# Kernel tuning notes

Measured on AMD Instinct MI355X. Metric: run time of the kernel, lower is better.

The kernel has to match this reference:

```python
import jax, jax.numpy as jnp
import numpy as np

N_PTS = 1_000_000
RES = 512
RANK = 48
OUT = 32
INIT_SCALE = 0.1


def _plane_sample(plane, gx, gy):
    """Bilinear grid_sample, align_corners=True, border padding.
    plane: [R, Res, Res] (R=rank); gx, gy: [N] in [-1,1] -> [R, N]."""
    res = plane.shape[-1]
    px = jnp.clip((gx + 1.0) * 0.5 * (res - 1), 0.0, res - 1.0)
    py = jnp.clip((gy + 1.0) * 0.5 * (res - 1), 0.0, res - 1.0)
    x0 = jnp.floor(px).astype(jnp.int32)
    y0 = jnp.floor(py).astype(jnp.int32)
    x1 = jnp.minimum(x0 + 1, res - 1)
    y1 = jnp.minimum(y0 + 1, res - 1)
    wx = px - x0.astype(px.dtype)
    wy = py - y0.astype(py.dtype)
    # gathers: [R, N] each
    v00 = plane[:, y0, x0]
    v01 = plane[:, y0, x1]
    v10 = plane[:, y1, x0]
    v11 = plane[:, y1, x1]
    return (v00 * (1 - wy) * (1 - wx) + v01 * (1 - wy) * wx
            + v10 * wy * (1 - wx) + v11 * wy * wx)


def _line_sample(line, gy):
    """Line is [R, Res] (width dim of size 1 collapses; x coord is 0 -> px=0).
    1-D linear interp along Res with gy in [-1,1] -> [R, N]."""
    res = line.shape[-1]
    py = jnp.clip((gy + 1.0) * 0.5 * (res - 1), 0.0, res - 1.0)
    y0 = jnp.floor(py).astype(jnp.int32)
    y1 = jnp.minimum(y0 + 1, res - 1)
    wy = py - y0.astype(py.dtype)
    return line[:, y0] * (1 - wy) + line[:, y1] * wy


def _geo_forward(coordinates, plane_xy, plane_xz, plane_yz,
                 line_z, line_y, line_x, proj_w, proj_b):
    coords = coordinates * 2.0 - 1.0  # [N, 3] in [-1, 1]
    cx, cy, cz = coords[:, 0], coords[:, 1], coords[:, 2]
    vm = (_plane_sample(plane_xy, cx, cy) * _line_sample(line_z, cz)
          + _plane_sample(plane_xz, cx, cz) * _line_sample(line_y, cy)
          + _plane_sample(plane_yz, cy, cz) * _line_sample(line_x, cx))  # [R, N]
    # projection: [N, R] @ [R, OUT] + b
    return vm.T @ proj_w.T + proj_b


def setup_inputs() -> dict:
    key = jax.random.key(0)
    ks = jax.random.split(key, 9)
    return {
        "coordinates": jax.random.uniform(ks[0], (N_PTS, 3), dtype=jnp.float32),
        "plane_xy": jax.random.normal(ks[1], (RANK, RES, RES), jnp.float32) * INIT_SCALE,
        "plane_xz": jax.random.normal(ks[2], (RANK, RES, RES), jnp.float32) * INIT_SCALE,
        "plane_yz": jax.random.normal(ks[3], (RANK, RES, RES), jnp.float32) * INIT_SCALE,
        "line_z": jax.random.normal(ks[4], (RANK, RES), jnp.float32) * INIT_SCALE,
        "line_y": jax.random.normal(ks[5], (RANK, RES), jnp.float32) * INIT_SCALE,
        "line_x": jax.random.normal(ks[6], (RANK, RES), jnp.float32) * INIT_SCALE,
        "proj_w": jax.random.normal(ks[7], (OUT, RANK), jnp.float32) * INIT_SCALE,
        "proj_b": jnp.zeros((OUT,), jnp.float32),
    }


def reference(coordinates, plane_xy, plane_xz, plane_yz,
              line_z, line_y, line_x, proj_w, proj_b):
    return _geo_forward(coordinates, plane_xy, plane_xz, plane_yz,
                        line_z, line_y, line_x, proj_w, proj_b)
```

## Files before the change

### kernel.cpp

```cpp
#include <hip/hip_runtime.h>
#include <stdint.h>

#define RES      512
#define TEXELS   (RES * RES)
#define NPTS     1000000
#define RANK     48
#define ODIM     32
#define PPB      64
#define VMS      52
#define OSTR     33
#define TT       128
#define TS       25
#define CELLS    32768

typedef unsigned int u32;
typedef float vf4 __attribute__((ext_vector_type(4)));

__device__ __forceinline__ float lobf(u32 u) { return __uint_as_float(u << 16); }
__device__ __forceinline__ float hibf(u32 u) { return __uint_as_float(u & 0xffff0000u); }

__device__ __forceinline__ float ntl(const float* p) {
    return __builtin_nontemporal_load(p);
}
__device__ __forceinline__ u32 ntlu(const u32* p) {
    return __builtin_nontemporal_load(p);
}

__device__ __forceinline__ u32 pkbf(float a, float b) {
    u32 x = __float_as_uint(a), y = __float_as_uint(b);
    u32 xr = (x + 0x7fffu + ((x >> 16) & 1u)) >> 16;
    u32 yr = (y + 0x7fffu + ((y >> 16) & 1u)) & 0xffff0000u;
    return xr | yr;
}

__device__ __forceinline__ u32 sprd5(u32 a) {
    a &= 31u;
    a = (a | (a << 8)) & 0x100Fu;
    a = (a | (a << 4)) & 0x10C3u;
    a = (a | (a << 2)) & 0x1249u;
    return a;
}
__device__ __forceinline__ u32 cellOf(float x, float y, float z) {
    u32 cx = (u32)fminf(fmaxf(x * 32.f, 0.f), 31.f);
    u32 cy = (u32)fminf(fmaxf(y * 32.f, 0.f), 31.f);
    u32 cz = (u32)fminf(fmaxf(z * 32.f, 0.f), 31.f);
    return sprd5(cx) | (sprd5(cy) << 1) | (sprd5(cz) << 2);
}

template <int TEXB>
__global__ __launch_bounds__(256) void transpose_planes(
    const float* __restrict__ p0, const float* __restrict__ p1,
    const float* __restrict__ p2, char* __restrict__ ws)
{
    __shared__ u32 lds[TT * TS + 8];

    int t = threadIdx.x;
    int base = blockIdx.x * TT;
    int plane = blockIdx.y;
    const float* src = (plane == 0) ? p0 : ((plane == 1) ? p1 : p2);

    int t7 = t & (TT - 1);
    int half = t >> 7;
#pragma unroll
    for (int j = 0; j < 12; ++j) {
        int d = half * 12 + j;
        float a = ntl(&src[(size_t)(2 * d) * TEXELS + base + t7]);
        float b = ntl(&src[(size_t)(2 * d + 1) * TEXELS + base + t7]);
        lds[t7 * TS + d] = pkbf(a, b);
    }
    __syncthreads();

    char* outp = ws + (size_t)plane * TEXELS * TEXB + (size_t)base * TEXB;
    constexpr int NS = TT * TEXB / (16 * 256);
#pragma unroll
    for (int s = 0; s < NS; ++s) {
        u32 o = (u32)(s * 256 + t) * 16u;
        u32 texel, rem;
        if (TEXB == 128) { texel = o >> 7; rem = o & 127u; }
        else {
            texel = ((o >> 5) * 43691u) >> 17;
            rem = o - texel * 96u;
        }
        u32 dw = texel * TS + (rem >> 2);
        uint4 q = make_uint4(lds[dw], lds[dw + 1], lds[dw + 2], lds[dw + 3]);
        *(uint4*)(outp + o) = q;
    }
}

template <int TEXB>
__global__ __launch_bounds__(256) void transpose_lines(
    const float* __restrict__ lz, const float* __restrict__ ly,
    const float* __restrict__ lx, char* __restrict__ ws)
{
    int id = blockIdx.x * 256 + threadIdx.x;
    int line = id >> 9;
    int pos = id & (RES - 1);
    const float* src = (line == 0) ? lz : ((line == 1) ? ly : lx);
    char* dst = ws + (size_t)3 * TEXELS * TEXB + (size_t)line * RES * TEXB
                   + (size_t)pos * TEXB;
#pragma unroll
    for (int k = 0; k < 6; ++k) {
        uint4 q;
        q.x = pkbf(ntl(&src[(8 * k + 0) * RES + pos]), ntl(&src[(8 * k + 1) * RES + pos]));
        q.y = pkbf(ntl(&src[(8 * k + 2) * RES + pos]), ntl(&src[(8 * k + 3) * RES + pos]));
        q.z = pkbf(ntl(&src[(8 * k + 4) * RES + pos]), ntl(&src[(8 * k + 5) * RES + pos]));
        q.w = pkbf(ntl(&src[(8 * k + 6) * RES + pos]), ntl(&src[(8 * k + 7) * RES + pos]));
        *(uint4*)(dst + 16 * k) = q;
    }
}

__global__ __launch_bounds__(256) void zero_counts(u32* __restrict__ counts) {
    counts[blockIdx.x * 256 + threadIdx.x] = 0u;
}

__global__ __launch_bounds__(256) void cell_count(
    const float* __restrict__ coords, u32* __restrict__ counts)
{
    int pt = blockIdx.x * 256 + threadIdx.x;
    if (pt >= NPTS) return;
    float x = ntl(&coords[3 * pt + 0]);
    float y = ntl(&coords[3 * pt + 1]);
    float z = ntl(&coords[3 * pt + 2]);
    atomicAdd(&counts[cellOf(x, y, z)], 1u);
}

__global__ __launch_bounds__(1024) void cell_scan(
    const u32* __restrict__ counts, u32* __restrict__ cursors)
{
    __shared__ u32 wt[16];
    int t = threadIdx.x;
    u32 local[32];
    u32 s = 0;
#pragma unroll
    for (int i = 0; i < 32; ++i) {
        local[i] = s;
        s += counts[t * 32 + i];
    }
    u32 tot = s;
    int lane = t & 63, w = t >> 6;
    u32 incl = tot;
#pragma unroll
    for (int d = 1; d < 64; d <<= 1) {
        u32 v = __shfl_up(incl, d);
        if (lane >= d) incl += v;
    }
    if (lane == 63) wt[w] = incl;
    __syncthreads();
    if (t == 0) {
        u32 a = 0;
#pragma unroll
        for (int i = 0; i < 16; ++i) { u32 x = wt[i]; wt[i] = a; a += x; }
    }
    __syncthreads();
    u32 base = wt[w] + (incl - tot);
#pragma unroll
    for (int i = 0; i < 32; ++i)
        cursors[t * 32 + i] = base + local[i];
}

__global__ __launch_bounds__(256) void cell_scatter(
    const float* __restrict__ coords, u32* __restrict__ cursors,
    u32* __restrict__ perm, float* __restrict__ rc)
{
    int pt = blockIdx.x * 256 + threadIdx.x;
    if (pt >= NPTS) return;
    float x = ntl(&coords[3 * pt + 0]);
    float y = ntl(&coords[3 * pt + 1]);
    float z = ntl(&coords[3 * pt + 2]);
    u32 pos = atomicAdd(&cursors[cellOf(x, y, z)], 1u);
    perm[pos] = (u32)pt;
    rc[3 * pos + 0] = x;
    rc[3 * pos + 1] = y;
    rc[3 * pos + 2] = z;
}

__device__ __forceinline__ void prep1(float g, int& i0, int& i1, float& w) {
    float p = fminf(fmaxf((g + 1.f) * 0.5f * 511.f, 0.f), 511.f);
    float fp = floorf(p);
    i0 = (int)fp;
    i1 = min(i0 + 1, RES - 1);
    w = p - fp;
}

template <int TEXB, bool SORTED>
__global__ __launch_bounds__(512, 4) void geo_main(
    const float* __restrict__ coords, const char* __restrict__ ws,
    const u32* __restrict__ perm,
    const float* __restrict__ W, const float* __restrict__ Bb,
    float* __restrict__ out)
{
    __shared__ float vm_lds[PPB * VMS];
    __shared__ u32 opt_lds[PPB];

    int tid = threadIdx.x;
    int ptL = tid >> 3;
    int c = tid & 7;

    int bid = blockIdx.x;
    if (SORTED) {
        int nwg = gridDim.x;
        int q = nwg >> 3, r = nwg & 7;
        int xcd = bid & 7, slot = bid >> 3;
        bid = (xcd < r ? xcd * (q + 1) : r * (q + 1) + (xcd - r) * q) + slot;
    }
    int pt = bid * PPB + ptL;

    float gx = ntl(&coords[3 * pt + 0]) * 2.f - 1.f;
    float gy = ntl(&coords[3 * pt + 1]) * 2.f - 1.f;
    float gz = ntl(&coords[3 * pt + 2]) * 2.f - 1.f;

    if (c == 0)
        opt_lds[ptL] = SORTED ? ntlu(&perm[pt]) : (u32)pt;

    int x0, x1, y0, y1, z0, z1;
    float wx, wy, wz;
    prep1(gx, x0, x1, wx);
    prep1(gy, y0, y1, wy);
    prep1(gz, z0, z1, wz);

    const size_t PW = (size_t)TEXELS * TEXB;
    const size_t LW = (size_t)RES * TEXB;
    const char* pxy = ws;
    const char* pxz = ws + PW;
    const char* pyz = ws + 2 * PW;
    const char* lzb = ws + 3 * PW;
    const char* lyb = lzb + LW;
    const char* lxb = lyb + LW;

    u32 co = 12u * (u32)c;

    u32 q[12][3], le[3][3], lf[3][3];
    {
        u32 offs[12];
        offs[0] = (u32)(y0 * RES + x0) * TEXB + co;
        offs[1] = (u32)(y0 * RES + x1) * TEXB + co;
        offs[2] = (u32)(y1 * RES + x0) * TEXB + co;
        offs[3] = (u32)(y1 * RES + x1) * TEXB + co;
        offs[4] = (u32)(z0 * RES + x0) * TEXB + co;
        offs[5] = (u32)(z0 * RES + x1) * TEXB + co;
        offs[6] = (u32)(z1 * RES + x0) * TEXB + co;
        offs[7] = (u32)(z1 * RES + x1) * TEXB + co;
        offs[8]  = (u32)(z0 * RES + y0) * TEXB + co;
        offs[9]  = (u32)(z0 * RES + y1) * TEXB + co;
        offs[10] = (u32)(z1 * RES + y0) * TEXB + co;
        offs[11] = (u32)(z1 * RES + y1) * TEXB + co;
        const char* bases[3] = { pxy, pxz, pyz };
#pragma unroll
        for (int p = 0; p < 3; ++p) {
#pragma unroll
            for (int k = 0; k < 4; ++k) {
                const u32* s = (const u32*)(bases[p] + offs[4 * p + k]);
                q[4 * p + k][0] = s[0];
                q[4 * p + k][1] = s[1];
                q[4 * p + k][2] = s[2];
            }
        }
        const char* lb[3] = { lzb, lyb, lxb };
        u32 l0[3] = { (u32)z0 * TEXB + co, (u32)y0 * TEXB + co, (u32)x0 * TEXB + co };
        u32 l1[3] = { (u32)z1 * TEXB + co, (u32)y1 * TEXB + co, (u32)x1 * TEXB + co };
#pragma unroll
        for (int p = 0; p < 3; ++p) {
            const u32* s0 = (const u32*)(lb[p] + l0[p]);
            const u32* s1 = (const u32*)(lb[p] + l1[p]);
            le[p][0] = s0[0]; le[p][1] = s0[1]; le[p][2] = s0[2];
            lf[p][0] = s1[0]; lf[p][1] = s1[1]; lf[p][2] = s1[2];
        }
    }

    float pw[3][4];
    pw[0][0] = (1.f - wy) * (1.f - wx); pw[0][1] = (1.f - wy) * wx;
    pw[0][2] = wy * (1.f - wx);         pw[0][3] = wy * wx;
    pw[1][0] = (1.f - wz) * (1.f - wx); pw[1][1] = (1.f - wz) * wx;
    pw[1][2] = wz * (1.f - wx);         pw[1][3] = wz * wx;
    pw[2][0] = (1.f - wz) * (1.f - wy); pw[2][1] = (1.f - wz) * wy;
    pw[2][2] = wz * (1.f - wy);         pw[2][3] = wz * wy;
    float lw[3] = { wz, wy, wx };

    float vm[6] = { 0.f, 0.f, 0.f, 0.f, 0.f, 0.f };
#pragma unroll
    for (int p = 0; p < 3; ++p) {
        float s0 = pw[p][0], s1 = pw[p][1], s2 = pw[p][2], s3 = pw[p][3];
        float il = 1.f - lw[p], wl = lw[p];
#pragma unroll
        for (int d = 0; d < 3; ++d) {
            u32 a = q[4 * p + 0][d], b = q[4 * p + 1][d];
            u32 cc = q[4 * p + 2][d], dd = q[4 * p + 3][d];
            float slo = s0 * lobf(a) + s1 * lobf(b) + s2 * lobf(cc) + s3 * lobf(dd);
            float shi = s0 * hibf(a) + s1 * hibf(b) + s2 * hibf(cc) + s3 * hibf(dd);
            float llo = il * lobf(le[p][d]) + wl * lobf(lf[p][d]);
            float lhi = il * hibf(le[p][d]) + wl * hibf(lf[p][d]);
            vm[2 * d + 0] = fmaf(slo, llo, vm[2 * d + 0]);
            vm[2 * d + 1] = fmaf(shi, lhi, vm[2 * d + 1]);
        }
    }

    float* vr = vm_lds + ptL * VMS + 6 * c;
    *(float2*)(vr + 0) = make_float2(vm[0], vm[1]);
    *(float2*)(vr + 2) = make_float2(vm[2], vm[3]);
    *(float2*)(vr + 4) = make_float2(vm[4], vm[5]);

    __syncthreads();

    int wav = __builtin_amdgcn_readfirstlane(tid >> 6);
    int lane = tid & 63;
    int ob = wav * 4;

    const float* vmrow = vm_lds + lane * VMS;
    float4 bb = *(const float4*)(Bb + ob);
    float a0 = bb.x, a1 = bb.y, a2 = bb.z, a3 = bb.w;
#pragma unroll 4
    for (int k = 0; k < 12; ++k) {
        float4 v = *(const float4*)(vmrow + 4 * k);
        float4 w0 = *(const float4*)(W + (ob + 0) * RANK + 4 * k);
        float4 w1 = *(const float4*)(W + (ob + 1) * RANK + 4 * k);
        float4 w2 = *(const float4*)(W + (ob + 2) * RANK + 4 * k);
        float4 w3 = *(const float4*)(W + (ob + 3) * RANK + 4 * k);
        a0 = fmaf(v.x, w0.x, a0); a0 = fmaf(v.y, w0.y, a0);
        a0 = fmaf(v.z, w0.z, a0); a0 = fmaf(v.w, w0.w, a0);
        a1 = fmaf(v.x, w1.x, a1); a1 = fmaf(v.y, w1.y, a1);
        a1 = fmaf(v.z, w1.z, a1); a1 = fmaf(v.w, w1.w, a1);
        a2 = fmaf(v.x, w2.x, a2); a2 = fmaf(v.y, w2.y, a2);
        a2 = fmaf(v.z, w2.z, a2); a2 = fmaf(v.w, w2.w, a2);
        a3 = fmaf(v.x, w3.x, a3); a3 = fmaf(v.y, w3.y, a3);
        a3 = fmaf(v.z, w3.z, a3); a3 = fmaf(v.w, w3.w, a3);
    }

    __syncthreads();
    {
        vf4 r; r.x = a0; r.y = a1; r.z = a2; r.w = a3;
        *(vf4*)(vm_lds + lane * OSTR + ob) = r;
    }
    __syncthreads();
    {
        int p8 = lane >> 3;
        int c2 = lane & 7;
        int gp = wav * 8 + p8;
        vf4 v = *(const vf4*)(vm_lds + gp * OSTR + 4 * c2);
        size_t orow = (size_t)opt_lds[gp];
        __builtin_nontemporal_store(v, (vf4*)(out + orow * ODIM + 4 * c2));
    }
}

template <int TEXB>
static void launch_unsorted(const float* coords, const float* pxy, const float* pxz,
                            const float* pyz, const float* lz, const float* ly,
                            const float* lx, const float* W, const float* Bb,
                            float* out, char* ws, hipStream_t stream) {
    dim3 gt(TEXELS / TT, 3);
    transpose_planes<TEXB><<<gt, 256, 0, stream>>>(pxy, pxz, pyz, ws);
    transpose_lines<TEXB><<<6, 256, 0, stream>>>(lz, ly, lx, ws);
    geo_main<TEXB, false><<<NPTS / PPB, 512, 0, stream>>>(coords, ws, nullptr, W, Bb, out);
}

extern "C" void kernel_launch(void* const* d_in, const int* in_sizes, int n_in,
                              void* d_out, int out_size, void* d_ws, size_t ws_size,
                              hipStream_t stream) {
    const float* coords = (const float*)d_in[0];
    const float* pxy = (const float*)d_in[1];
    const float* pxz = (const float*)d_in[2];
    const float* pyz = (const float*)d_in[3];
    const float* lz = (const float*)d_in[4];
    const float* ly = (const float*)d_in[5];
    const float* lx = (const float*)d_in[6];
    const float* W = (const float*)d_in[7];
    const float* Bb = (const float*)d_in[8];
    float* out = (float*)d_out;
    char* ws = (char*)d_ws;

    size_t pool96 = (size_t)3 * TEXELS * 96 + (size_t)3 * RES * 96;
    size_t o_counts = (pool96 + 255) & ~(size_t)255;
    size_t o_cursors = o_counts + (size_t)CELLS * 4;
    size_t o_perm = o_cursors + (size_t)CELLS * 4;
    size_t o_rc = o_perm + (size_t)NPTS * 4;
    size_t need_sorted = o_rc + (size_t)NPTS * 12;
    size_t need128 = (size_t)3 * TEXELS * 128 + (size_t)3 * RES * 128;
    size_t need96 = pool96;

    if (ws_size >= need_sorted) {
        u32* counts = (u32*)(ws + o_counts);
        u32* cursors = (u32*)(ws + o_cursors);
        u32* perm = (u32*)(ws + o_perm);
        float* rc = (float*)(ws + o_rc);

        dim3 gt(TEXELS / TT, 3);
        transpose_planes<96><<<gt, 256, 0, stream>>>(pxy, pxz, pyz, ws);
        transpose_lines<96><<<6, 256, 0, stream>>>(lz, ly, lx, ws);
        zero_counts<<<CELLS / 256, 256, 0, stream>>>(counts);
        cell_count<<<(NPTS + 255) / 256, 256, 0, stream>>>(coords, counts);
        cell_scan<<<1, 1024, 0, stream>>>(counts, cursors);
        cell_scatter<<<(NPTS + 255) / 256, 256, 0, stream>>>(coords, cursors, perm, rc);
        geo_main<96, true><<<NPTS / PPB, 512, 0, stream>>>(rc, ws, perm, W, Bb, out);
    } else if (ws_size >= need128) {
        launch_unsorted<128>(coords, pxy, pxz, pyz, lz, ly, lx, W, Bb, out, ws, stream);
    } else {
        launch_unsorted<96>(coords, pxy, pxz, pyz, lz, ly, lx, W, Bb, out, ws, stream);
    }
}
```

Measured before the change: 483.3 us.

## Fuse preprocessing kernels and overlap plane transpose with sort passes

Merges the plane transpose, line transpose, cell count, scan and scatter into three heterogeneous kernels. The transpose tiles are split across them so the transpose work runs alongside the latency-bound count, scan and scatter passes. The separate perm array and 12-byte coordinate buffer become one 16-byte record (xyz plus the original index), read with a single vector load in the main kernel. The zeroing kernel becomes a memset, the scan uses a single 256-thread block, and transpose loads are widened to float4. Launch count drops, at the cost of more complex kernels and a 16-byte rather than 12-byte workspace record per point.

After: 463.4 us. -4.1%, faster.

```diff
diff --git a/kernel.cpp b/kernel.cpp
--- a/kernel.cpp
+++ b/kernel.cpp
@@ -12,6 +12,11 @@
 #define TT       128
 #define TS       25
 #define CELLS    32768
+#define TPALL    6144
+#define TPA      2560
+#define TPB      512
+#define TPC      3072
+#define CNTB     3907
 
 typedef unsigned int u32;
 typedef float vf4 __attribute__((ext_vector_type(4)));
@@ -22,8 +27,8 @@
 __device__ __forceinline__ float ntl(const float* p) {
     return __builtin_nontemporal_load(p);
 }
-__device__ __forceinline__ u32 ntlu(const u32* p) {
-    return __builtin_nontemporal_load(p);
+__device__ __forceinline__ vf4 ntl4(const float* p) {
+    return __builtin_nontemporal_load((const vf4*)p);
 }
 
 __device__ __forceinline__ u32 pkbf(float a, float b) {
@@ -47,57 +52,48 @@
     return sprd5(cx) | (sprd5(cy) << 1) | (sprd5(cz) << 2);
 }
 
-template <int TEXB>
-__global__ __launch_bounds__(256) void transpose_planes(
+__device__ __forceinline__ void tp_role(int bx, int t,
     const float* __restrict__ p0, const float* __restrict__ p1,
-    const float* __restrict__ p2, char* __restrict__ ws)
-{
-    __shared__ u32 lds[TT * TS + 8];
-
-    int t = threadIdx.x;
-    int base = blockIdx.x * TT;
-    int plane = blockIdx.y;
+    const float* __restrict__ p2, char* __restrict__ ws, u32* lds)
+{
+    int tile = bx & 2047;
+    int plane = bx >> 11;
     const float* src = (plane == 0) ? p0 : ((plane == 1) ? p1 : p2);
-
-    int t7 = t & (TT - 1);
-    int half = t >> 7;
-#pragma unroll
-    for (int j = 0; j < 12; ++j) {
-        int d = half * 12 + j;
-        float a = ntl(&src[(size_t)(2 * d) * TEXELS + base + t7]);
-        float b = ntl(&src[(size_t)(2 * d + 1) * TEXELS + base + t7]);
-        lds[t7 * TS + d] = pkbf(a, b);
-    }
-    __syncthreads();
-
-    char* outp = ws + (size_t)plane * TEXELS * TEXB + (size_t)base * TEXB;
-    constexpr int NS = TT * TEXB / (16 * 256);
-#pragma unroll
-    for (int s = 0; s < NS; ++s) {
+    int base = tile * TT;
+    int xi = t & 31, dg = t >> 5;
+#pragma unroll
+    for (int j = 0; j < 3; ++j) {
+        int d = dg + 8 * j;
+        vf4 a = ntl4(src + (size_t)(2 * d) * TEXELS + base + 4 * xi);
+        vf4 b = ntl4(src + (size_t)(2 * d + 1) * TEXELS + base + 4 * xi);
+        lds[(4 * xi + 0) * TS + d] = pkbf(a.x, b.x);
+        lds[(4 * xi + 1) * TS + d] = pkbf(a.y, b.y);
+        lds[(4 * xi + 2) * TS + d] = pkbf(a.z, b.z);
+        lds[(4 * xi + 3) * TS + d] = pkbf(a.w, b.w);
+    }
+    __syncthreads();
+    char* outp = ws + (size_t)plane * TEXELS * 96 + (size_t)base * 96;
+#pragma unroll
+    for (int s = 0; s < 3; ++s) {
         u32 o = (u32)(s * 256 + t) * 16u;
-        u32 texel, rem;
-        if (TEXB == 128) { texel = o >> 7; rem = o & 127u; }
-        else {
-            texel = ((o >> 5) * 43691u) >> 17;
-            rem = o - texel * 96u;
-        }
+        u32 texel = ((o >> 5) * 43691u) >> 17;
+        u32 rem = o - texel * 96u;
         u32 dw = texel * TS + (rem >> 2);
         uint4 q = make_uint4(lds[dw], lds[dw + 1], lds[dw + 2], lds[dw + 3]);
         *(uint4*)(outp + o) = q;
     }
 }
 
-template <int TEXB>
-__global__ __launch_bounds__(256) void transpose_lines(
+__device__ __forceinline__ void lines_role(int lbx, int t,
     const float* __restrict__ lz, const float* __restrict__ ly,
     const float* __restrict__ lx, char* __restrict__ ws)
 {
-    int id = blockIdx.x * 256 + threadIdx.x;
+    int id = lbx * 256 + t;
     int line = id >> 9;
     int pos = id & (RES - 1);
     const float* src = (line == 0) ? lz : ((line == 1) ? ly : lx);
-    char* dst = ws + (size_t)3 * TEXELS * TEXB + (size_t)line * RES * TEXB
-                   + (size_t)pos * TEXB;
+    char* dst = ws + (size_t)3 * TEXELS * 96 + (size_t)line * RES * 96
+                   + (size_t)pos * 96;
 #pragma unroll
     for (int k = 0; k < 6; ++k) {
         uint4 q;
@@ -109,14 +105,10 @@
     }
 }
 
-__global__ __launch_bounds__(256) void zero_counts(u32* __restrict__ counts) {
-    counts[blockIdx.x * 256 + threadIdx.x] = 0u;
-}
-
-__global__ __launch_bounds__(256) void cell_count(
+__device__ __forceinline__ void count_role(int cbx, int t,
     const float* __restrict__ coords, u32* __restrict__ counts)
 {
-    int pt = blockIdx.x * 256 + threadIdx.x;
+    int pt = cbx * 256 + t;
     if (pt >= NPTS) return;
     float x = ntl(&coords[3 * pt + 0]);
     float y = ntl(&coords[3 * pt + 1]);
@@ -124,54 +116,138 @@
     atomicAdd(&counts[cellOf(x, y, z)], 1u);
 }
 
-__global__ __launch_bounds__(1024) void cell_scan(
-    const u32* __restrict__ counts, u32* __restrict__ cursors)
-{
-    __shared__ u32 wt[16];
-    int t = threadIdx.x;
-    u32 local[32];
-    u32 s = 0;
-#pragma unroll
-    for (int i = 0; i < 32; ++i) {
-        local[i] = s;
-        s += counts[t * 32 + i];
-    }
-    u32 tot = s;
-    int lane = t & 63, w = t >> 6;
+__device__ __forceinline__ void scan_role(int t,
+    const u32* __restrict__ counts, u32* __restrict__ cursors, u32* wt)
+{
+    const u32* cp = counts + t * 128;
+    u32 tot = 0;
+#pragma unroll 16
+    for (int i = 0; i < 128; ++i) tot += cp[i];
+    int lane = t & 63;
     u32 incl = tot;
 #pragma unroll
-    for (int d = 1; d < 64; d <<= 1) {
-        u32 v = __shfl_up(incl, d);
-        if (lane >= d) incl += v;
-    }
+    for (int d2 = 1; d2 < 64; d2 <<= 1) {
+        u32 v = __shfl_up(incl, d2);
+        if (lane >= d2) incl += v;
+    }
+    int w = t >> 6;
     if (lane == 63) wt[w] = incl;
     __syncthreads();
-    if (t == 0) {
-        u32 a = 0;
-#pragma unroll
-        for (int i = 0; i < 16; ++i) { u32 x = wt[i]; wt[i] = a; a += x; }
-    }
-    __syncthreads();
-    u32 base = wt[w] + (incl - tot);
-#pragma unroll
-    for (int i = 0; i < 32; ++i)
-        cursors[t * 32 + i] = base + local[i];
-}
-
-__global__ __launch_bounds__(256) void cell_scatter(
+    u32 run = incl - tot;
+#pragma unroll
+    for (int i = 0; i < 4; ++i) run += (i < w) ? wt[i] : 0u;
+    u32* op = cursors + t * 128;
+#pragma unroll 16
+    for (int i = 0; i < 128; ++i) { u32 c2 = cp[i]; op[i] = run; run += c2; }
+}
+
+__device__ __forceinline__ void scatter_role(int cbx, int t,
     const float* __restrict__ coords, u32* __restrict__ cursors,
-    u32* __restrict__ perm, float* __restrict__ rc)
-{
-    int pt = blockIdx.x * 256 + threadIdx.x;
+    vf4* __restrict__ rc2)
+{
+    int pt = cbx * 256 + t;
     if (pt >= NPTS) return;
     float x = ntl(&coords[3 * pt + 0]);
     float y = ntl(&coords[3 * pt + 1]);
     float z = ntl(&coords[3 * pt + 2]);
     u32 pos = atomicAdd(&cursors[cellOf(x, y, z)], 1u);
-    perm[pos] = (u32)pt;
-    rc[3 * pos + 0] = x;
-    rc[3 * pos + 1] = y;
-    rc[3 * pos + 2] = z;
+    vf4 v; v.x = x; v.y = y; v.z = z; v.w = __uint_as_float((u32)pt);
+    rc2[pos] = v;
+}
+
+__global__ __launch_bounds__(256) void k1_count_tp(
+    const float* __restrict__ coords, u32* __restrict__ counts,
+    const float* __restrict__ p0, const float* __restrict__ p1,
+    const float* __restrict__ p2, char* __restrict__ ws)
+{
+    __shared__ u32 lds[TT * TS + 8];
+    int bx = blockIdx.x, t = threadIdx.x;
+    if (bx < CNTB) count_role(bx, t, coords, counts);
+    else tp_role(bx - CNTB, t, p0, p1, p2, ws, lds);
+}
+
+__global__ __launch_bounds__(256) void k2_scan_lines_tp(
+    const u32* __restrict__ counts, u32* __restrict__ cursors,
+    const float* __restrict__ lz, const float* __restrict__ ly,
+    const float* __restrict__ lx,
+    const float* __restrict__ p0, const float* __restrict__ p1,
+    const float* __restrict__ p2, char* __restrict__ ws)
+{
+    __shared__ u32 lds[TT * TS + 8];
+    int bx = blockIdx.x, t = threadIdx.x;
+    if (bx == 0) scan_role(t, counts, cursors, lds);
+    else if (bx <= 6) lines_role(bx - 1, t, lz, ly, lx, ws);
+    else tp_role(bx - 7 + TPA, t, p0, p1, p2, ws, lds);
+}
+
+__global__ __launch_bounds__(256) void k3_scatter_tp(
+    const float* __restrict__ coords, u32* __restrict__ cursors,
+    vf4* __restrict__ rc2,
+    const float* __restrict__ p0, const float* __restrict__ p1,
+    const float* __restrict__ p2, char* __restrict__ ws)
+{
+    __shared__ u32 lds[TT * TS + 8];
+    int bx = blockIdx.x, t = threadIdx.x;
+    if (bx < CNTB) scatter_role(bx, t, coords, cursors, rc2);
+    else tp_role(bx - CNTB + TPA + TPB, t, p0, p1, p2, ws, lds);
+}
+
+template <int TEXB>
+__global__ __launch_bounds__(256) void transpose_planes(
+    const float* __restrict__ p0, const float* __restrict__ p1,
+    const float* __restrict__ p2, char* __restrict__ ws)
+{
+    __shared__ u32 lds[TT * TS + 8];
+    int t = threadIdx.x;
+    int base = blockIdx.x * TT;
+    int plane = blockIdx.y;
+    const float* src = (plane == 0) ? p0 : ((plane == 1) ? p1 : p2);
+    int xi = t & 31, dg = t >> 5;
+#pragma unroll
+    for (int j = 0; j < 3; ++j) {
+        int d = dg + 8 * j;
+        vf4 a = ntl4(src + (size_t)(2 * d) * TEXELS + base + 4 * xi);
+        vf4 b = ntl4(src + (size_t)(2 * d + 1) * TEXELS + base + 4 * xi);
+        lds[(4 * xi + 0) * TS + d] = pkbf(a.x, b.x);
+        lds[(4 * xi + 1) * TS + d] = pkbf(a.y, b.y);
+        lds[(4 * xi + 2) * TS + d] = pkbf(a.z, b.z);
+        lds[(4 * xi + 3) * TS + d] = pkbf(a.w, b.w);
+    }
+    __syncthreads();
+    char* outp = ws + (size_t)plane * TEXELS * TEXB + (size_t)base * TEXB;
+    constexpr int NS = TT * TEXB / (16 * 256);
+#pragma unroll
+    for (int s = 0; s < NS; ++s) {
+        u32 o = (u32)(s * 256 + t) * 16u;
+        u32 texel, rem;
+        if (TEXB == 128) { texel = o >> 7; rem = o & 127u; }
+        else { texel = ((o >> 5) * 43691u) >> 17; rem = o - texel * 96u; }
+        u32 dw = texel * TS + (rem >> 2);
+        uint4 q = make_uint4(lds[dw], lds[dw + 1], lds[dw + 2], lds[dw + 3]);
+        *(uint4*)(outp + o) = q;
+    }
+}
+
+template <int TEXB>
+__global__ __launch_bounds__(256) void transpose_lines(
+    const float* __restrict__ lz, const float* __restrict__ ly,
+    const float* __restrict__ lx, char* __restrict__ ws)
+{
+    int id = blockIdx.x * 256 + threadIdx.x;
+    int line = id >> 9;
+    int pos = id & (RES - 1);
+    const float* src = (line == 0) ? lz : ((line == 1) ? ly : lx);
+    char* dst = ws + (size_t)3 * TEXELS * TEXB + (size_t)line * RES * TEXB
+                   + (size_t)pos * TEXB;
+#pragma unroll
+    for (int k = 0; k < 6; ++k) {
+        uint4 q;
+        q.x = pkbf(ntl(&src[(8 * k + 0) * RES + pos]), ntl(&src[(8 * k + 1) * RES + pos]));
+        q.y = pkbf(ntl(&src[(8 * k + 2) * RES + pos]), ntl(&src[(8 * k + 3) * RES + pos]));
+        q.z = pkbf(ntl(&src[(8 * k + 4) * RES + pos]), ntl(&src[(8 * k + 5) * RES + pos]));
+        q.w = pkbf(ntl(&src[(8 * k + 6) * RES + pos]), ntl(&src[(8 * k + 7) * RES + pos]));
+        *(uint4*)(dst + 16 * k) = q;
+    }
 }
 
 __device__ __forceinline__ void prep1(float g, int& i0, int& i1, float& w) {
@@ -184,8 +260,7 @@
 
 template <int TEXB, bool SORTED>
 __global__ __launch_bounds__(512, 4) void geo_main(
-    const float* __restrict__ coords, const char* __restrict__ ws,
-    const u32* __restrict__ perm,
+    const void* __restrict__ cin, const char* __restrict__ ws,
     const float* __restrict__ W, const float* __restrict__ Bb,
     float* __restrict__ out)
 {
@@ -205,12 +280,20 @@
     }
     int pt = bid * PPB + ptL;
 
-    float gx = ntl(&coords[3 * pt + 0]) * 2.f - 1.f;
-    float gy = ntl(&coords[3 * pt + 1]) * 2.f - 1.f;
-    float gz = ntl(&coords[3 * pt + 2]) * 2.f - 1.f;
-
-    if (c == 0)
-        opt_lds[ptL] = SORTED ? ntlu(&perm[pt]) : (u32)pt;
+    float gx, gy, gz;
+    if (SORTED) {
+        vf4 cc = __builtin_nontemporal_load((const vf4*)cin + pt);
+        gx = cc.x * 2.f - 1.f;
+        gy = cc.y * 2.f - 1.f;
+        gz = cc.z * 2.f - 1.f;
+        if (c == 0) opt_lds[ptL] = __float_as_uint(cc.w);
+    } else {
+        const float* coords = (const float*)cin;
+        gx = ntl(&coords[3 * pt + 0]) * 2.f - 1.f;
+        gy = ntl(&coords[3 * pt + 1]) * 2.f - 1.f;
+        gz = ntl(&coords[3 * pt + 2]) * 2.f - 1.f;
+        if (c == 0) opt_lds[ptL] = (u32)pt;
+    }
 
     int x0, x1, y0, y1, z0, z1;
     float wx, wy, wz;
@@ -349,7 +432,7 @@
     dim3 gt(TEXELS / TT, 3);
     transpose_planes<TEXB><<<gt, 256, 0, stream>>>(pxy, pxz, pyz, ws);
     transpose_lines<TEXB><<<6, 256, 0, stream>>>(lz, ly, lx, ws);
-    geo_main<TEXB, false><<<NPTS / PPB, 512, 0, stream>>>(coords, ws, nullptr, W, Bb, out);
+    geo_main<TEXB, false><<<NPTS / PPB, 512, 0, stream>>>(coords, ws, W, Bb, out);
 }
 
 extern "C" void kernel_launch(void* const* d_in, const int* in_sizes, int n_in,
@@ -370,26 +453,24 @@
     size_t pool96 = (size_t)3 * TEXELS * 96 + (size_t)3 * RES * 96;
     size_t o_counts = (pool96 + 255) & ~(size_t)255;
     size_t o_cursors = o_counts + (size_t)CELLS * 4;
-    size_t o_perm = o_cursors + (size_t)CELLS * 4;
-    size_t o_rc = o_perm + (size_t)NPTS * 4;
-    size_t need_sorted = o_rc + (size_t)NPTS * 12;
+    size_t o_rc2 = o_cursors + (size_t)CELLS * 4;
+    size_t need_sorted = o_rc2 + (size_t)NPTS * 16;
     size_t need128 = (size_t)3 * TEXELS * 128 + (size_t)3 * RES * 128;
-    size_t need96 = pool96;
 
     if (ws_size >= need_sorted) {
         u32* counts = (u32*)(ws + o_counts);
         u32* cursors = (u32*)(ws + o_cursors);
-        u32* perm = (u32*)(ws + o_perm);
-        float* rc = (float*)(ws + o_rc);
-
-        dim3 gt(TEXELS / TT, 3);
-        transpose_planes<96><<<gt, 256, 0, stream>>>(pxy, pxz, pyz, ws);
-        transpose_lines<96><<<6, 256, 0, stream>>>(lz, ly, lx, ws);
-        zero_counts<<<CELLS / 256, 256, 0, stream>>>(counts);
-        cell_count<<<(NPTS + 255) / 256, 256, 0, stream>>>(coords, counts);
-        cell_scan<<<1, 1024, 0, stream>>>(counts, cursors);
-        cell_scatter<<<(NPTS + 255) / 256, 256, 0, stream>>>(coords, cursors, perm, rc);
-        geo_main<96, true><<<NPTS / PPB, 512, 0, stream>>>(rc, ws, perm, W, Bb, out);
+        vf4* rc2 = (vf4*)(ws + o_rc2);
+
+        hipMemsetAsync(counts, 0, (size_t)CELLS * 4, stream);
+        k1_count_tp<<<CNTB + TPA, 256, 0, stream>>>(coords, counts,
+                                                    pxy, pxz, pyz, ws);
+        k2_scan_lines_tp<<<7 + TPB, 256, 0, stream>>>(counts, cursors,
+                                                      lz, ly, lx,
+                                                      pxy, pxz, pyz, ws);
+        k3_scatter_tp<<<CNTB + TPC, 256, 0, stream>>>(coords, cursors, rc2,
+                                                      pxy, pxz, pyz, ws);
+        geo_main<96, true><<<NPTS / PPB, 512, 0, stream>>>(rc2, ws, W, Bb, out);
     } else if (ws_size >= need128) {
         launch_unsorted<128>(coords, pxy, pxz, pyz, lz, ly, lx, W, Bb, out, ws, stream);
     } else {
```

## Fuse prep kernels and pack sorted coords with point index

Applied to the files above, without the earlier changes.

The plane transpose, line transpose and cell counting are merged into one heterogeneous kernel whose blocks take different roles, so these independent preprocessing steps run concurrently and need fewer launches. The plane transpose no longer stages through LDS; each thread gathers 48 channels of one texel directly. The scatter writes a single 16-byte record (xyz plus original index) instead of separate perm and coordinate arrays, so the main kernel reads one vector load per point. Zeroing is done with a memset, and the 128-byte layout path is removed. Risks: the uncoalesced per-texel transpose reads and grid-stride loops could cost more than the saved launch overhead.

Result: no change. 474.8 us (-1.7%).

```diff
diff --git a/kernel.cpp b/kernel.cpp
--- a/kernel.cpp
+++ b/kernel.cpp
@@ -9,9 +9,11 @@
 #define PPB      64
 #define VMS      52
 #define OSTR     33
-#define TT       128
-#define TS       25
 #define CELLS    32768
+#define LINB     6
+#define CNTB     256
+#define TPB      1536
+#define SCTB     1024
 
 typedef unsigned int u32;
 typedef float vf4 __attribute__((ext_vector_type(4)));
@@ -20,9 +22,6 @@
 __device__ __forceinline__ float hibf(u32 u) { return __uint_as_float(u & 0xffff0000u); }
 
 __device__ __forceinline__ float ntl(const float* p) {
-    return __builtin_nontemporal_load(p);
-}
-__device__ __forceinline__ u32 ntlu(const u32* p) {
     return __builtin_nontemporal_load(p);
 }
 
@@ -47,57 +46,44 @@
     return sprd5(cx) | (sprd5(cy) << 1) | (sprd5(cz) << 2);
 }
 
-template <int TEXB>
-__global__ __launch_bounds__(256) void transpose_planes(
+__device__ __forceinline__ void tp_one(int g,
     const float* __restrict__ p0, const float* __restrict__ p1,
     const float* __restrict__ p2, char* __restrict__ ws)
 {
-    __shared__ u32 lds[TT * TS + 8];
-
-    int t = threadIdx.x;
-    int base = blockIdx.x * TT;
-    int plane = blockIdx.y;
+    int plane = g >> 18;
+    int texel = g & (TEXELS - 1);
     const float* src = (plane == 0) ? p0 : ((plane == 1) ? p1 : p2);
-
-    int t7 = t & (TT - 1);
-    int half = t >> 7;
-#pragma unroll
-    for (int j = 0; j < 12; ++j) {
-        int d = half * 12 + j;
-        float a = ntl(&src[(size_t)(2 * d) * TEXELS + base + t7]);
-        float b = ntl(&src[(size_t)(2 * d + 1) * TEXELS + base + t7]);
-        lds[t7 * TS + d] = pkbf(a, b);
-    }
-    __syncthreads();
-
-    char* outp = ws + (size_t)plane * TEXELS * TEXB + (size_t)base * TEXB;
-    constexpr int NS = TT * TEXB / (16 * 256);
-#pragma unroll
-    for (int s = 0; s < NS; ++s) {
-        u32 o = (u32)(s * 256 + t) * 16u;
-        u32 texel, rem;
-        if (TEXB == 128) { texel = o >> 7; rem = o & 127u; }
-        else {
-            texel = ((o >> 5) * 43691u) >> 17;
-            rem = o - texel * 96u;
-        }
-        u32 dw = texel * TS + (rem >> 2);
-        uint4 q = make_uint4(lds[dw], lds[dw + 1], lds[dw + 2], lds[dw + 3]);
-        *(uint4*)(outp + o) = q;
-    }
-}
-
-template <int TEXB>
-__global__ __launch_bounds__(256) void transpose_lines(
+    u32 c2[24];
+#pragma unroll
+    for (int h = 0; h < 2; ++h) {
+        float fa[12], fb[12];
+#pragma unroll
+        for (int d = 0; d < 12; ++d) {
+            fa[d] = ntl(src + (size_t)(2 * (h * 12 + d) + 0) * TEXELS + texel);
+            fb[d] = ntl(src + (size_t)(2 * (h * 12 + d) + 1) * TEXELS + texel);
+        }
+#pragma unroll
+        for (int d = 0; d < 12; ++d) c2[h * 12 + d] = pkbf(fa[d], fb[d]);
+    }
+    char* dst = ws + (size_t)plane * TEXELS * 96 + (size_t)texel * 96;
+#pragma unroll
+    for (int s = 0; s < 6; ++s) {
+        uint4 q = make_uint4(c2[4 * s + 0], c2[4 * s + 1],
+                             c2[4 * s + 2], c2[4 * s + 3]);
+        *(uint4*)(dst + 16 * s) = q;
+    }
+}
+
+__device__ __forceinline__ void lines_role(int j, int t,
     const float* __restrict__ lz, const float* __restrict__ ly,
     const float* __restrict__ lx, char* __restrict__ ws)
 {
-    int id = blockIdx.x * 256 + threadIdx.x;
+    int id = j * 256 + t;
     int line = id >> 9;
     int pos = id & (RES - 1);
     const float* src = (line == 0) ? lz : ((line == 1) ? ly : lx);
-    char* dst = ws + (size_t)3 * TEXELS * TEXB + (size_t)line * RES * TEXB
-                   + (size_t)pos * TEXB;
+    char* dst = ws + (size_t)3 * TEXELS * 96 + (size_t)line * RES * 96
+                   + (size_t)pos * 96;
 #pragma unroll
     for (int k = 0; k < 6; ++k) {
         uint4 q;
@@ -109,22 +95,31 @@
     }
 }
 
-__global__ __launch_bounds__(256) void zero_counts(u32* __restrict__ counts) {
-    counts[blockIdx.x * 256 + threadIdx.x] = 0u;
-}
-
-__global__ __launch_bounds__(256) void cell_count(
-    const float* __restrict__ coords, u32* __restrict__ counts)
-{
-    int pt = blockIdx.x * 256 + threadIdx.x;
-    if (pt >= NPTS) return;
-    float x = ntl(&coords[3 * pt + 0]);
-    float y = ntl(&coords[3 * pt + 1]);
-    float z = ntl(&coords[3 * pt + 2]);
-    atomicAdd(&counts[cellOf(x, y, z)], 1u);
-}
-
-__global__ __launch_bounds__(1024) void cell_scan(
+__global__ __launch_bounds__(256) void k1_prep(
+    const float* __restrict__ coords, u32* __restrict__ counts,
+    const float* __restrict__ p0, const float* __restrict__ p1,
+    const float* __restrict__ p2,
+    const float* __restrict__ lz, const float* __restrict__ ly,
+    const float* __restrict__ lx, char* __restrict__ ws)
+{
+    int bx = blockIdx.x, t = threadIdx.x;
+    if (bx < LINB) {
+        lines_role(bx, t, lz, ly, lx, ws);
+    } else if (bx < LINB + CNTB) {
+        for (int idx = (bx - LINB) * 256 + t; idx < NPTS; idx += CNTB * 256) {
+            float x = ntl(&coords[3 * idx + 0]);
+            float y = ntl(&coords[3 * idx + 1]);
+            float z = ntl(&coords[3 * idx + 2]);
+            atomicAdd(&counts[cellOf(x, y, z)], 1u);
+        }
+    } else {
+        int w = bx - LINB - CNTB;
+        for (int g = w * 256 + t; g < 3 * TEXELS; g += TPB * 256)
+            tp_one(g, p0, p1, p2, ws);
+    }
+}
+
+__global__ __launch_bounds__(1024) void k2_scan(
     const u32* __restrict__ counts, u32* __restrict__ cursors)
 {
     __shared__ u32 wt[16];
@@ -158,20 +153,33 @@
         cursors[t * 32 + i] = base + local[i];
 }
 
-__global__ __launch_bounds__(256) void cell_scatter(
+__global__ __launch_bounds__(256) void k3_scatter(
     const float* __restrict__ coords, u32* __restrict__ cursors,
-    u32* __restrict__ perm, float* __restrict__ rc)
-{
-    int pt = blockIdx.x * 256 + threadIdx.x;
-    if (pt >= NPTS) return;
-    float x = ntl(&coords[3 * pt + 0]);
-    float y = ntl(&coords[3 * pt + 1]);
-    float z = ntl(&coords[3 * pt + 2]);
-    u32 pos = atomicAdd(&cursors[cellOf(x, y, z)], 1u);
-    perm[pos] = (u32)pt;
-    rc[3 * pos + 0] = x;
-    rc[3 * pos + 1] = y;
-    rc[3 * pos + 2] = z;
+    vf4* __restrict__ rc2)
+{
+    int t = threadIdx.x;
+    for (int idx = blockIdx.x * 256 + t; idx < NPTS; idx += SCTB * 256) {
+        float x = ntl(&coords[3 * idx + 0]);
+        float y = ntl(&coords[3 * idx + 1]);
+        float z = ntl(&coords[3 * idx + 2]);
+        u32 pos = atomicAdd(&cursors[cellOf(x, y, z)], 1u);
+        vf4 v; v.x = x; v.y = y; v.z = z; v.w = __uint_as_float((u32)idx);
+        __builtin_nontemporal_store(v, rc2 + pos);
+    }
+}
+
+__global__ __launch_bounds__(256) void tp_stream_only(
+    const float* __restrict__ p0, const float* __restrict__ p1,
+    const float* __restrict__ p2, char* __restrict__ ws)
+{
+    int g = blockIdx.x * 256 + threadIdx.x;
+    tp_one(g, p0, p1, p2, ws);
+}
+__global__ __launch_bounds__(256) void lines_only(
+    const float* __restrict__ lz, const float* __restrict__ ly,
+    const float* __restrict__ lx, char* __restrict__ ws)
+{
+    lines_role(blockIdx.x, threadIdx.x, lz, ly, lx, ws);
 }
 
 __device__ __forceinline__ void prep1(float g, int& i0, int& i1, float& w) {
@@ -184,8 +192,7 @@
 
 template <int TEXB, bool SORTED>
 __global__ __launch_bounds__(512, 4) void geo_main(
-    const float* __restrict__ coords, const char* __restrict__ ws,
-    const u32* __restrict__ perm,
+    const void* __restrict__ cin, const char* __restrict__ ws,
     const float* __restrict__ W, const float* __restrict__ Bb,
     float* __restrict__ out)
 {
@@ -205,12 +212,20 @@
     }
     int pt = bid * PPB + ptL;
 
-    float gx = ntl(&coords[3 * pt + 0]) * 2.f - 1.f;
-    float gy = ntl(&coords[3 * pt + 1]) * 2.f - 1.f;
-    float gz = ntl(&coords[3 * pt + 2]) * 2.f - 1.f;
-
-    if (c == 0)
-        opt_lds[ptL] = SORTED ? ntlu(&perm[pt]) : (u32)pt;
+    float gx, gy, gz;
+    if (SORTED) {
+        vf4 cc = __builtin_nontemporal_load((const vf4*)cin + pt);
+        gx = cc.x * 2.f - 1.f;
+        gy = cc.y * 2.f - 1.f;
+        gz = cc.z * 2.f - 1.f;
+        if (c == 0) opt_lds[ptL] = __float_as_uint(cc.w);
+    } else {
+        const float* coords = (const float*)cin;
+        gx = ntl(&coords[3 * pt + 0]) * 2.f - 1.f;
+        gy = ntl(&coords[3 * pt + 1]) * 2.f - 1.f;
+        gz = ntl(&coords[3 * pt + 2]) * 2.f - 1.f;
+        if (c == 0) opt_lds[ptL] = (u32)pt;
+    }
 
     int x0, x1, y0, y1, z0, z1;
     float wx, wy, wz;
@@ -341,17 +356,6 @@
     }
 }
 
-template <int TEXB>
-static void launch_unsorted(const float* coords, const float* pxy, const float* pxz,
-                            const float* pyz, const float* lz, const float* ly,
-                            const float* lx, const float* W, const float* Bb,
-                            float* out, char* ws, hipStream_t stream) {
-    dim3 gt(TEXELS / TT, 3);
-    transpose_planes<TEXB><<<gt, 256, 0, stream>>>(pxy, pxz, pyz, ws);
-    transpose_lines<TEXB><<<6, 256, 0, stream>>>(lz, ly, lx, ws);
-    geo_main<TEXB, false><<<NPTS / PPB, 512, 0, stream>>>(coords, ws, nullptr, W, Bb, out);
-}
-
 extern "C" void kernel_launch(void* const* d_in, const int* in_sizes, int n_in,
                               void* d_out, int out_size, void* d_ws, size_t ws_size,
                               hipStream_t stream) {
@@ -370,29 +374,24 @@
     size_t pool96 = (size_t)3 * TEXELS * 96 + (size_t)3 * RES * 96;
     size_t o_counts = (pool96 + 255) & ~(size_t)255;
     size_t o_cursors = o_counts + (size_t)CELLS * 4;
-    size_t o_perm = o_cursors + (size_t)CELLS * 4;
-    size_t o_rc = o_perm + (size_t)NPTS * 4;
-    size_t need_sorted = o_rc + (size_t)NPTS * 12;
-    size_t need128 = (size_t)3 * TEXELS * 128 + (size_t)3 * RES * 128;
-    size_t need96 = pool96;
+    size_t o_rc2 = o_cursors + (size_t)CELLS * 4;
+    size_t need_sorted = o_rc2 + (size_t)NPTS * 16;
 
     if (ws_size >= need_sorted) {
         u32* counts = (u32*)(ws + o_counts);
         u32* cursors = (u32*)(ws + o_cursors);
-        u32* perm = (u32*)(ws + o_perm);
-        float* rc = (float*)(ws + o_rc);
-
-        dim3 gt(TEXELS / TT, 3);
-        transpose_planes<96><<<gt, 256, 0, stream>>>(pxy, pxz, pyz, ws);
-        transpose_lines<96><<<6, 256, 0, stream>>>(lz, ly, lx, ws);
-        zero_counts<<<CELLS / 256, 256, 0, stream>>>(counts);
-        cell_count<<<(NPTS + 255) / 256, 256, 0, stream>>>(coords, counts);
-        cell_scan<<<1, 1024, 0, stream>>>(counts, cursors);
-        cell_scatter<<<(NPTS + 255) / 256, 256, 0, stream>>>(coords, cursors, perm, rc);
-        geo_main<96, true><<<NPTS / PPB, 512, 0, stream>>>(rc, ws, perm, W, Bb, out);
-    } else if (ws_size >= need128) {
-        launch_unsorted<128>(coords, pxy, pxz, pyz, lz, ly, lx, W, Bb, out, ws, stream);
+        vf4* rc2 = (vf4*)(ws + o_rc2);
+
+        hipMemsetAsync(counts, 0, (size_t)CELLS * 4, stream);
+        k1_prep<<<LINB + CNTB + TPB, 256, 0, stream>>>(coords, counts,
+                                                       pxy, pxz, pyz,
+                                                       lz, ly, lx, ws);
+        k2_scan<<<1, 1024, 0, stream>>>(counts, cursors);
+        k3_scatter<<<SCTB, 256, 0, stream>>>(coords, cursors, rc2);
+        geo_main<96, true><<<NPTS / PPB, 512, 0, stream>>>(rc2, ws, W, Bb, out);
     } else {
-        launch_unsorted<96>(coords, pxy, pxz, pyz, lz, ly, lx, W, Bb, out, ws, stream);
-    }
-}
+        tp_stream_only<<<3 * TEXELS / 256, 256, 0, stream>>>(pxy, pxz, pyz, ws);
+        lines_only<<<6, 256, 0, stream>>>(lz, ly, lx, ws);
+        geo_main<96, false><<<NPTS / PPB, 512, 0, stream>>>(coords, ws, W, Bb, out);
+    }
+}
```
